# Optimization experiments

Hardware: AMD Instinct MI355X
Metric: run time of the kernel (lower is better)

The kernel has to match this reference:

```python
import jax, jax.numpy as jnp
import numpy as np

B, T, F_DIM, HID, CH = 16, 4096, 47, 64, 256  # batch, frames, feature_dim, hidden_feature_dim, num_channels


def setup_inputs() -> dict:
    key = jax.random.key(0)
    ks = jax.random.split(key, 8)
    s = 0.08  # weight scale
    return {
        "features": jax.random.normal(ks[0], (B, T, F_DIM), jnp.float32),
        # conv1: Conv1d(47, 64, k=1) -> pointwise linear, torch weight (out,in,1) squeezed
        "W1": jax.random.normal(ks[1], (HID, F_DIM), jnp.float32) * s,
        "b1": jnp.zeros((HID,), jnp.float32),
        # conv2: Conv1d(256, 256, k=2), torch weight (out, in, k)
        "W2": jax.random.normal(ks[2], (CH, 4 * HID, 2), jnp.float32) * s,
        "b2": jnp.zeros((CH,), jnp.float32),
        # tconv: ConvTranspose1d(256, 256, k=4, stride=4), torch weight (in, out, k)
        "Wt": jax.random.normal(ks[3], (CH, CH, 4), jnp.float32) * s,
        "bt": jnp.zeros((CH,), jnp.float32),
        # GRU(256, 256), torch layout: (3*H, in) with gate order [r, z, n]
        "W_ih": jax.random.normal(ks[4], (3 * CH, CH), jnp.float32) * s,
        "W_hh": jax.random.normal(ks[5], (3 * CH, CH), jnp.float32) * s,
        "b_ih": jnp.zeros((3 * CH,), jnp.float32),
        "b_hh": jnp.zeros((3 * CH,), jnp.float32),
    }


def reference(features, W1, b1, W2, b2, Wt, bt, W_ih, W_hh, b_ih, b_hh):
    b, t = features.shape[0], features.shape[1]
    ch = Wt.shape[1]
    # conv1 (k=1) == pointwise linear + tanh: (B,T,47) -> (B,T,64)
    c = jnp.tanh(jnp.einsum('btf,hf->bth', features, W1) + b1)
    # group 4 frames: (B, T/4, 256)
    c = c.reshape(b, t // 4, -1)
    # conv2 k=2 with left pad 1 (causal): y[t] = W2[..0] x[t-1] + W2[..1] x[t]
    cp = jnp.pad(c, ((0, 0), (1, 0), (0, 0)))
    c = jnp.tanh(jnp.einsum('bti,oi->bto', cp[:, :-1], W2[:, :, 0])
                 + jnp.einsum('bti,oi->bto', cp[:, 1:], W2[:, :, 1]) + b2)
    # tconv: stride-4 transpose conv, k=4 -> each frame emits 4 steps
    c = jnp.tanh(jnp.einsum('bti,iok->btko', c, Wt) + bt)  # (B, T/4, 4, CH)
    c = c.reshape(b, t, ch)
    # GRU (torch semantics, gate order r,z,n); precompute input projections
    gates_x = jnp.einsum('btc,gc->btg', c, W_ih) + b_ih  # (B,T,3CH)

    def step(h, gx):
        gh = h @ W_hh.T + b_hh
        xr, xz, xn = jnp.split(gx, 3, axis=-1)
        hr, hz, hn = jnp.split(gh, 3, axis=-1)
        r = jax.nn.sigmoid(xr + hr)
        z = jax.nn.sigmoid(xz + hz)
        n = jnp.tanh(xn + r * hn)
        h = (1 - z) * n + z * h
        return h, h

    h0 = jnp.zeros((b, ch), features.dtype)
    _, hs = jax.lax.scan(step, h0, jnp.swapaxes(gates_x, 0, 1))  # (T,B,CH)
    return jnp.swapaxes(hs, 0, 1)  # (B,T,CH)
```

## Files before the change

kernel.cpp:

```cpp
#include <hip/hip_runtime.h>
#include <hip/hip_bf16.h>
#include <stdint.h>

#define B_   16
#define T_   4096
#define F_   47
#define HID_ 64
#define CH_  256
#define TG_  1024
#define G3_  768

using bf16x8 = __attribute__((ext_vector_type(8))) short;
using f32x4  = __attribute__((ext_vector_type(4))) float;
using f16x8  = __attribute__((ext_vector_type(8))) _Float16;

__device__ __forceinline__ short f2bf(float f) {
    union { float f; uint32_t u; } v; v.f = f;
    uint32_t u = v.u;
    uint32_t r = (u + 0x7fffu + ((u >> 16) & 1u)) >> 16;
    return (short)r;
}
__device__ __forceinline__ float bf2f(short s) {
    union { uint32_t u; float f; } v; v.u = ((uint32_t)(uint16_t)s) << 16;
    return v.f;
}
__device__ __forceinline__ float fast_tanh(float x) {
    float e = __expf(2.f * x);
    return 1.f - 2.f / (e + 1.f);
}
__device__ __forceinline__ float fast_sigmoid(float x) {
    return 1.f / (1.f + __expf(-x));
}

#if __has_builtin(__builtin_amdgcn_global_load_lds)
#define HAS_GLL 1
__device__ __forceinline__ void gl_lds16(const void* g, void* l) {
    __builtin_amdgcn_global_load_lds(
        (const __attribute__((address_space(1))) uint32_t*)g,
        (__attribute__((address_space(3))) uint32_t*)l, 16, 0, 0);
}
#else
#define HAS_GLL 0
#endif

__global__ __launch_bounds__(256) void k1_conv1(const float* __restrict__ feat,
        const float* __restrict__ W1, const float* __restrict__ b1,
        short* __restrict__ c1) {
    __shared__ float sW[47 * 64];
    __shared__ float sF[4 * 47];
    int tid = threadIdx.x;
    int b = blockIdx.x >> 10, t0 = (blockIdx.x & 1023) * 4;
    if (tid < 188) sF[tid] = feat[((size_t)b * T_ + t0) * 47 + tid];
    for (int i = tid; i < 47 * 64; i += 256) {
        int f = i >> 6, h = i & 63;
        sW[i] = W1[h * 47 + f];
    }
    __syncthreads();
    int fr = tid >> 6, h = tid & 63;
    float acc = b1[h];
    #pragma unroll
    for (int f = 0; f < 47; ++f)
        acc += sF[fr * 47 + f] * sW[f * 64 + h];
    c1[((size_t)b * T_ + t0 + fr) * 64 + h] = f2bf(fast_tanh(acc));
}

__global__ __launch_bounds__(256) void k_prep(const float* __restrict__ W2,
        const float* __restrict__ Wt, const float* __restrict__ Wih_f,
        short* __restrict__ W2t, short* __restrict__ Wtt, short* __restrict__ Wih) {
    int idx = blockIdx.x * 256 + threadIdx.x;
    if (idx < 256 * 512) {
        int o = idx >> 9, i = idx & 511, d = i >> 8, jj = i & 255;
        W2t[idx] = f2bf(W2[(size_t)o * 512 + jj * 2 + d]);
    }
    {
        int n = idx >> 8, ic = idx & 255, o = n & 255, kp = n >> 8;
        Wtt[idx] = f2bf(Wt[(size_t)ic * 1024 + o * 4 + kp]);
    }
    if (idx < G3_ * CH_)
        Wih[idx] = f2bf(Wih_f[idx]);
}

__global__ __launch_bounds__(256) void k2_conv2(const short* __restrict__ c1,
        const short* __restrict__ W2t, const float* __restrict__ b2,
        short* __restrict__ y2) {
    int tid = threadIdx.x, w = tid >> 6, l = tid & 63;
    int lane16 = l & 15, quad = l >> 4;
    int mt = blockIdx.x * 4 + w;
    int row = mt * 16 + lane16;
    int tg = row & 1023;
    const short* Arow = c1 + (size_t)row * 256 - 256;
    bf16x8 zero8 = {0,0,0,0,0,0,0,0};
    bf16x8 af[16];
    #pragma unroll
    for (int kt = 0; kt < 16; ++kt) {
        int i0 = kt * 32 + quad * 8;
        bool masked = (tg == 0) && (kt < 8);
        const short* p = masked ? c1 : (Arow + i0);
        bf16x8 v = *(const bf16x8*)p;
        af[kt] = masked ? zero8 : v;
    }
    #pragma unroll
    for (int nt = 0; nt < 16; ++nt) {
        int n = nt * 16 + lane16;
        f32x4 acc = {0.f, 0.f, 0.f, 0.f};
        const short* Brow = W2t + (size_t)n * 512 + quad * 8;
        #pragma unroll
        for (int kt = 0; kt < 16; ++kt) {
            bf16x8 bf = *(const bf16x8*)(Brow + kt * 32);
            acc = __builtin_amdgcn_mfma_f32_16x16x32_bf16(af[kt], bf, acc, 0, 0, 0);
        }
        float bias = b2[n];
        #pragma unroll
        for (int r = 0; r < 4; ++r) {
            int mrow = mt * 16 + quad * 4 + r;
            y2[(size_t)mrow * 256 + n] = f2bf(fast_tanh(acc[r] + bias));
        }
    }
}

__global__ __launch_bounds__(256) void k3a_tconv(const short* __restrict__ y2,
        const short* __restrict__ Wtt, const float* __restrict__ bt,
        short* __restrict__ c3) {
    int tid = threadIdx.x, w = tid >> 6, l = tid & 63;
    int lane16 = l & 15, quad = l >> 4;
    int mt = blockIdx.x;
    int row = mt * 16 + lane16;
    const short* Arow = y2 + (size_t)row * 256 + quad * 8;
    bf16x8 af[8];
    #pragma unroll
    for (int kt = 0; kt < 8; ++kt) af[kt] = *(const bf16x8*)(Arow + kt * 32);
    #pragma unroll
    for (int nt2 = 0; nt2 < 16; ++nt2) {
        int n = (w * 16 + nt2) * 16 + lane16;
        f32x4 acc = {0.f, 0.f, 0.f, 0.f};
        const short* Brow = Wtt + (size_t)n * 256 + quad * 8;
        #pragma unroll
        for (int kt = 0; kt < 8; ++kt) {
            bf16x8 bf = *(const bf16x8*)(Brow + kt * 32);
            acc = __builtin_amdgcn_mfma_f32_16x16x32_bf16(af[kt], bf, acc, 0, 0, 0);
        }
        int kp = n >> 8, o = n & 255;
        float bias = bt[o];
        #pragma unroll
        for (int r = 0; r < 4; ++r) {
            int mrow = mt * 16 + quad * 4 + r;
            int bb = mrow >> 10, tgg = mrow & 1023;
            c3[(((size_t)bb * TG_ + tgg) * 4 + kp) * 256 + o] =
                f2bf(fast_tanh(acc[r] + bias));
        }
    }
}

__global__ __launch_bounds__(256) void k3b_xproj(const short* __restrict__ c3,
        const short* __restrict__ Wih, const float* __restrict__ b_ih,
        short* __restrict__ gates) {
    int tid = threadIdx.x, w = tid >> 6, l = tid & 63;
    int lane16 = l & 15, quad = l >> 4;
    int mt = blockIdx.x;
    int row = mt * 16 + lane16;
    const short* Arow = c3 + (size_t)row * 256 + quad * 8;
    bf16x8 af[8];
    #pragma unroll
    for (int kt = 0; kt < 8; ++kt) af[kt] = *(const bf16x8*)(Arow + kt * 32);
    #pragma unroll
    for (int nt2 = 0; nt2 < 12; ++nt2) {
        int n = (w * 12 + nt2) * 16 + lane16;
        f32x4 acc = {0.f, 0.f, 0.f, 0.f};
        const short* Brow = Wih + (size_t)n * 256 + quad * 8;
        #pragma unroll
        for (int kt = 0; kt < 8; ++kt) {
            bf16x8 bf = *(const bf16x8*)(Brow + kt * 32);
            acc = __builtin_amdgcn_mfma_f32_16x16x32_bf16(af[kt], bf, acc, 0, 0, 0);
        }
        float bias = b_ih[n];
        #pragma unroll
        for (int r = 0; r < 4; ++r) {
            int mrow = mt * 16 + quad * 4 + r;
            gates[(size_t)mrow * G3_ + n] = f2bf(acc[r] + bias);
        }
    }
}

__global__ __launch_bounds__(512, 2) void k4_gru_mfma(const float* __restrict__ W_hh,
        const float* __restrict__ b_hh, const short* __restrict__ gates,
        float* __restrict__ out) {
    __shared__ __align__(16) short gxb[2][8][G3_];
    __shared__ __align__(16) float part[G3_];
    __shared__ __align__(16) float ob[8 * 256];
    __shared__ __align__(16) _Float16 h_s[256];

    int tid = threadIdx.x, l = tid & 63, w = tid >> 6;
    int lane16 = l & 15, quad = l >> 4;
    int b = blockIdx.x;

    f16x8 frag[6][8];
    #pragma unroll
    for (int mt = 0; mt < 6; ++mt) {
        const float* wrow = W_hh + (size_t)((w * 6 + mt) * 16 + lane16) * 256 + quad * 8;
        #pragma unroll
        for (int kt = 0; kt < 8; ++kt) {
            const float4* p = (const float4*)(wrow + kt * 32);
            float4 x = p[0], y = p[1];
            f16x8 f;
            f[0] = (_Float16)x.x; f[1] = (_Float16)x.y;
            f[2] = (_Float16)x.z; f[3] = (_Float16)x.w;
            f[4] = (_Float16)y.x; f[5] = (_Float16)y.y;
            f[6] = (_Float16)y.z; f[7] = (_Float16)y.w;
            frag[mt][kt] = f;
        }
    }

    float h_reg = 0.f, bhr = 0.f, bhz = 0.f, bhn = 0.f;
    if (tid < 256) {
        bhr = b_hh[tid]; bhz = b_hh[256 + tid]; bhn = b_hh[512 + tid];
        h_s[tid] = (_Float16)0.f;
    }

    const short* gbase = gates + (size_t)b * T_ * G3_;
    const char* gbytes = (const char*)gbase;

#if HAS_GLL
    {
        char* dst = (char*)&gxb[0][0][0];
        gl_lds16(gbytes + w * 1024 + l * 16, dst + w * 1024);
        if (w < 4) gl_lds16(gbytes + (8 + w) * 1024 + l * 16, dst + (8 + w) * 1024);
    }
#else
    {
        const uint32_t* g32 = (const uint32_t*)gbytes;
        uint32_t* d = (uint32_t*)&gxb[0][0][0];
        #pragma unroll
        for (int i = 0; i < 6; ++i) d[tid + i * 512] = g32[tid + i * 512];
    }
#endif
    __syncthreads();

    float* outb = out + (size_t)b * T_ * CH_;
    for (int s = 0; s < T_; ++s) {
        bool grp0 = ((s & 7) == 0) && (s + 8 < T_);
#if HAS_GLL
        if (grp0) {
            const char* src = gbytes + (size_t)(s + 8) * 1536;
            char* dst = (char*)&gxb[((s >> 3) + 1) & 1][0][0];
            gl_lds16(src + w * 1024 + l * 16, dst + w * 1024);
            if (w < 4) gl_lds16(src + (8 + w) * 1024 + l * 16, dst + (8 + w) * 1024);
        }
#else
        uint32_t pf[6];
        if (grp0) {
            const uint32_t* src = (const uint32_t*)(gbytes + (size_t)(s + 8) * 1536);
            #pragma unroll
            for (int i = 0; i < 6; ++i) pf[i] = src[tid + i * 512];
        }
#endif

        f32x4 acc[6];
        #pragma unroll
        for (int mt = 0; mt < 6; ++mt) acc[mt] = (f32x4){0.f, 0.f, 0.f, 0.f};
        #pragma unroll
        for (int kt = 0; kt < 8; ++kt) {
            f16x8 hb = *(const f16x8*)&h_s[kt * 32 + quad * 8];
            #pragma unroll
            for (int mt = 0; mt < 6; ++mt)
                acc[mt] = __builtin_amdgcn_mfma_f32_16x16x32_f16(frag[mt][kt], hb, acc[mt], 0, 0, 0);
        }
        if (lane16 == 0) {
            #pragma unroll
            for (int mt = 0; mt < 6; ++mt)
                *(f32x4*)&part[(w * 6 + mt) * 16 + quad * 4] = acc[mt];
        }
        __syncthreads();

#if !HAS_GLL
        if (grp0) {
            uint32_t* d = (uint32_t*)&gxb[((s >> 3) + 1) & 1][0][0];
            #pragma unroll
            for (int i = 0; i < 6; ++i) d[tid + i * 512] = pf[i];
        }
#endif
        if (tid < 256) {
            const short* gx = &gxb[(s >> 3) & 1][s & 7][0];
            float gr = part[tid];
            float gz = part[256 + tid];
            float gn = part[512 + tid];
            float xr = bf2f(gx[tid]), xz = bf2f(gx[256 + tid]), xn = bf2f(gx[512 + tid]);
            float r = fast_sigmoid(xr + gr + bhr);
            float z = fast_sigmoid(xz + gz + bhz);
            float nn = fast_tanh(xn + r * (gn + bhn));
            h_reg = (1.f - z) * nn + z * h_reg;
            h_s[tid] = (_Float16)h_reg;
            ob[(s & 7) * 256 + tid] = h_reg;
        }
        __syncthreads();

        if ((s & 7) == 7) {
            f32x4 v = *(const f32x4*)&ob[tid * 4];
            *(f32x4*)&outb[(size_t)(s - 7 + (tid >> 6)) * 256 + (tid & 63) * 4] = v;
        }
    }
}

extern "C" void kernel_launch(void* const* d_in, const int* in_sizes, int n_in,
                              void* d_out, int out_size, void* d_ws, size_t ws_size,
                              hipStream_t stream) {
    const float* feat  = (const float*)d_in[0];
    const float* W1    = (const float*)d_in[1];
    const float* b1    = (const float*)d_in[2];
    const float* W2    = (const float*)d_in[3];
    const float* b2    = (const float*)d_in[4];
    const float* Wt    = (const float*)d_in[5];
    const float* bt    = (const float*)d_in[6];
    const float* Wih_f = (const float*)d_in[7];
    const float* Whh   = (const float*)d_in[8];
    const float* bih   = (const float*)d_in[9];
    const float* bhh   = (const float*)d_in[10];
    float* out = (float*)d_out;

    char* ws = (char*)d_ws;
    short* c3    = (short*)(ws);
    short* c1    = (short*)(ws);
    short* gates = (short*)(ws + 33554432);
    short* y2    = (short*)(ws + 33554432);
    short* W2t   = (short*)(ws + 134217728);
    short* Wtt   = (short*)(ws + 134217728 + 262144);
    short* Wih   = (short*)(ws + 134217728 + 262144 + 524288);

    k1_conv1   <<<16384, 256, 0, stream>>>(feat, W1, b1, c1);
    k_prep     <<<1024, 256, 0, stream>>>(W2, Wt, Wih_f, W2t, Wtt, Wih);
    k2_conv2   <<<256,  256, 0, stream>>>(c1, W2t, b2, y2);
    k3a_tconv  <<<1024, 256, 0, stream>>>(y2, Wtt, bt, c3);
    k3b_xproj  <<<4096, 256, 0, stream>>>(c3, Wih, bih, gates);
    k4_gru_mfma<<<16,   512, 0, stream>>>(Whh, bhh, gates, out);
}
```

Before: 5.763 ms.

## Split GRU recurrent matvec between MFMA (r,z gates) and fdot2 (n gate)

The GRU step kernel now computes only the r and z gate rows of W_hh·h with MFMA, cutting per-wave MFMA tiles from 6 to 4. The n-gate rows are held in registers as packed half2 and computed with fdot2 over quarter-rows, then reduced across 4 lanes with DPP adds. The hidden state moves to a double-buffered, padded LDS layout to avoid bank conflicts and read/write races. The aim is to shorten the serial per-step critical path by splitting the work across MFMA and VALU. In exchange it raises register pressure, which matters at the 512-thread, 2-blocks-per-CU launch bound.

```diff
diff --git a/kernel.cpp b/kernel.cpp
--- a/kernel.cpp
+++ b/kernel.cpp
@@ -13,6 +13,7 @@
 using bf16x8 = __attribute__((ext_vector_type(8))) short;
 using f32x4  = __attribute__((ext_vector_type(4))) float;
 using f16x8  = __attribute__((ext_vector_type(8))) _Float16;
+using h2     = __attribute__((ext_vector_type(2))) _Float16;
 
 __device__ __forceinline__ short f2bf(float f) {
     union { float f; uint32_t u; } v; v.f = f;
@@ -30,6 +31,23 @@
 }
 __device__ __forceinline__ float fast_sigmoid(float x) {
     return 1.f / (1.f + __expf(-x));
+}
+
+#if __has_builtin(__builtin_amdgcn_fdot2)
+#define FDOT2(a, b, c) __builtin_amdgcn_fdot2((a), (b), (c), false)
+#else
+__device__ __forceinline__ float fdot2_emul(h2 a, h2 b, float c) {
+    return c + (float)a[0] * (float)b[0] + (float)a[1] * (float)b[1];
+}
+#define FDOT2(a, b, c) fdot2_emul((a), (b), (c))
+#endif
+
+template <int CTRL>
+__device__ __forceinline__ float dpp_add(float x) {
+    union { float f; int i; } a, b;
+    a.f = x;
+    b.i = __builtin_amdgcn_update_dpp(0, a.i, CTRL, 0xf, 0xf, true);
+    return x + b.f;
 }
 
 #if __has_builtin(__builtin_amdgcn_global_load_lds)
@@ -181,22 +199,23 @@
     }
 }
 
-__global__ __launch_bounds__(512, 2) void k4_gru_mfma(const float* __restrict__ W_hh,
+__global__ __launch_bounds__(512, 2) void k4_gru_hyb(const float* __restrict__ W_hh,
         const float* __restrict__ b_hh, const short* __restrict__ gates,
         float* __restrict__ out) {
     __shared__ __align__(16) short gxb[2][8][G3_];
     __shared__ __align__(16) float part[G3_];
     __shared__ __align__(16) float ob[8 * 256];
-    __shared__ __align__(16) _Float16 h_s[256];
+    __shared__ __align__(16) short hq_s[2][4 * 72];
 
     int tid = threadIdx.x, l = tid & 63, w = tid >> 6;
     int lane16 = l & 15, quad = l >> 4;
+    int q = tid & 3, i2 = tid >> 2;
     int b = blockIdx.x;
 
-    f16x8 frag[6][8];
-    #pragma unroll
-    for (int mt = 0; mt < 6; ++mt) {
-        const float* wrow = W_hh + (size_t)((w * 6 + mt) * 16 + lane16) * 256 + quad * 8;
+    f16x8 afrag[4][8];
+    #pragma unroll
+    for (int mt = 0; mt < 4; ++mt) {
+        const float* wrow = W_hh + (size_t)((w * 4 + mt) * 16 + lane16) * 256 + quad * 8;
         #pragma unroll
         for (int kt = 0; kt < 8; ++kt) {
             const float4* p = (const float4*)(wrow + kt * 32);
@@ -206,15 +225,27 @@
             f[2] = (_Float16)x.z; f[3] = (_Float16)x.w;
             f[4] = (_Float16)y.x; f[5] = (_Float16)y.y;
             f[6] = (_Float16)y.z; f[7] = (_Float16)y.w;
-            frag[mt][kt] = f;
+            afrag[mt][kt] = f;
+        }
+    }
+
+    h2 wreg[2][32];
+    #pragma unroll
+    for (int rr = 0; rr < 2; ++rr) {
+        const float2* row = (const float2*)(W_hh + (size_t)(512 + 2 * i2 + rr) * 256 + q * 64);
+        #pragma unroll
+        for (int j = 0; j < 32; ++j) {
+            float2 v = row[j];
+            h2 p; p[0] = (_Float16)v.x; p[1] = (_Float16)v.y;
+            wreg[rr][j] = p;
         }
     }
 
     float h_reg = 0.f, bhr = 0.f, bhz = 0.f, bhn = 0.f;
     if (tid < 256) {
         bhr = b_hh[tid]; bhz = b_hh[256 + tid]; bhn = b_hh[512 + tid];
-        h_s[tid] = (_Float16)0.f;
-    }
+    }
+    if (tid < 288) hq_s[0][tid] = 0;
 
     const short* gbase = gates + (size_t)b * T_ * G3_;
     const char* gbytes = (const char*)gbase;
@@ -254,20 +285,42 @@
         }
 #endif
 
-        f32x4 acc[6];
-        #pragma unroll
-        for (int mt = 0; mt < 6; ++mt) acc[mt] = (f32x4){0.f, 0.f, 0.f, 0.f};
+        f32x4 acc4[4];
+        #pragma unroll
+        for (int mt = 0; mt < 4; ++mt) acc4[mt] = (f32x4){0.f, 0.f, 0.f, 0.f};
         #pragma unroll
         for (int kt = 0; kt < 8; ++kt) {
-            f16x8 hb = *(const f16x8*)&h_s[kt * 32 + quad * 8];
-            #pragma unroll
-            for (int mt = 0; mt < 6; ++mt)
-                acc[mt] = __builtin_amdgcn_mfma_f32_16x16x32_f16(frag[mt][kt], hb, acc[mt], 0, 0, 0);
-        }
+            int k0 = kt * 32 + quad * 8;
+            f16x8 hb = *(const f16x8*)&hq_s[s & 1][(k0 >> 6) * 72 + (k0 & 63)];
+            #pragma unroll
+            for (int mt = 0; mt < 4; ++mt)
+                acc4[mt] = __builtin_amdgcn_mfma_f32_16x16x32_f16(afrag[mt][kt], hb, acc4[mt], 0, 0, 0);
+        }
+
+        float a0 = 0.f, a1 = 0.f;
+        const short* hb2 = &hq_s[s & 1][q * 72];
+        #pragma unroll
+        for (int g2 = 0; g2 < 8; ++g2) {
+            union { f16x8 v8; h2 p[4]; } hc;
+            hc.v8 = *(const f16x8*)(hb2 + g2 * 8);
+            #pragma unroll
+            for (int p2 = 0; p2 < 4; ++p2) {
+                h2 hv = hc.p[p2];
+                a0 = FDOT2(wreg[0][g2 * 4 + p2], hv, a0);
+                a1 = FDOT2(wreg[1][g2 * 4 + p2], hv, a1);
+            }
+        }
+        a0 = dpp_add<0xB1>(a0); a0 = dpp_add<0x4E>(a0);
+        a1 = dpp_add<0xB1>(a1); a1 = dpp_add<0x4E>(a1);
+
         if (lane16 == 0) {
             #pragma unroll
-            for (int mt = 0; mt < 6; ++mt)
-                *(f32x4*)&part[(w * 6 + mt) * 16 + quad * 4] = acc[mt];
+            for (int mt = 0; mt < 4; ++mt)
+                *(f32x4*)&part[(w * 4 + mt) * 16 + quad * 4] = acc4[mt];
+        }
+        if (q == 0) {
+            float2 nn2; nn2.x = a0; nn2.y = a1;
+            *(float2*)&part[512 + 2 * i2] = nn2;
         }
         __syncthreads();
 
@@ -288,7 +341,8 @@
             float z = fast_sigmoid(xz + gz + bhz);
             float nn = fast_tanh(xn + r * (gn + bhn));
             h_reg = (1.f - z) * nn + z * h_reg;
-            h_s[tid] = (_Float16)h_reg;
+            union { _Float16 f; short u; } cv; cv.f = (_Float16)h_reg;
+            hq_s[(s + 1) & 1][(tid >> 6) * 72 + (tid & 63)] = cv.u;
             ob[(s & 7) * 256 + tid] = h_reg;
         }
         __syncthreads();
@@ -325,10 +379,10 @@
     short* Wtt   = (short*)(ws + 134217728 + 262144);
     short* Wih   = (short*)(ws + 134217728 + 262144 + 524288);
 
-    k1_conv1   <<<16384, 256, 0, stream>>>(feat, W1, b1, c1);
-    k_prep     <<<1024, 256, 0, stream>>>(W2, Wt, Wih_f, W2t, Wtt, Wih);
-    k2_conv2   <<<256,  256, 0, stream>>>(c1, W2t, b2, y2);
-    k3a_tconv  <<<1024, 256, 0, stream>>>(y2, Wtt, bt, c3);
-    k3b_xproj  <<<4096, 256, 0, stream>>>(c3, Wih, bih, gates);
-    k4_gru_mfma<<<16,   512, 0, stream>>>(Whh, bhh, gates, out);
-}
+    k1_conv1  <<<16384, 256, 0, stream>>>(feat, W1, b1, c1);
+    k_prep    <<<1024, 256, 0, stream>>>(W2, Wt, Wih_f, W2t, Wtt, Wih);
+    k2_conv2  <<<256,  256, 0, stream>>>(c1, W2t, b2, y2);
+    k3a_tconv <<<1024, 256, 0, stream>>>(y2, Wtt, bt, c3);
+    k3b_xproj <<<4096, 256, 0, stream>>>(c3, Wih, bih, gates);
+    k4_gru_hyb<<<16,   512, 0, stream>>>(Whh, bhh, gates, out);
+}
```

Result: slower. 6.099 ms (+5.8%).

## Batch all 16 sequences into one GRU block using MFMA N dimension

Applied to the files above, without the earlier changes.

The GRU recurrence now runs in a single 512-thread block that puts the 16 batch elements in the MFMA N dimension, instead of one block per batch where the h vector filled every column. Each lane keeps its gate outputs in registers and applies the nonlinearity directly. This removes the LDS partial-sum round trip and one of the two barriers per step, and h is double-buffered in LDS. Gate inputs are now read straight from global memory every step with no prefetch, and outputs are stored every step, so global latency may land on the serial critical path.

```diff
diff --git a/kernel.cpp b/kernel.cpp
--- a/kernel.cpp
+++ b/kernel.cpp
@@ -11,6 +11,7 @@
 #define G3_  768
 
 using bf16x8 = __attribute__((ext_vector_type(8))) short;
+using bf16x4 = __attribute__((ext_vector_type(4))) short;
 using f32x4  = __attribute__((ext_vector_type(4))) float;
 using f16x8  = __attribute__((ext_vector_type(8))) _Float16;
 
@@ -31,17 +32,15 @@
 __device__ __forceinline__ float fast_sigmoid(float x) {
     return 1.f / (1.f + __expf(-x));
 }
-
-#if __has_builtin(__builtin_amdgcn_global_load_lds)
-#define HAS_GLL 1
-__device__ __forceinline__ void gl_lds16(const void* g, void* l) {
-    __builtin_amdgcn_global_load_lds(
-        (const __attribute__((address_space(1))) uint32_t*)g,
-        (__attribute__((address_space(3))) uint32_t*)l, 16, 0, 0);
-}
-#else
-#define HAS_GLL 0
-#endif
+__device__ __forceinline__ f16x8 cvt8(const float* p) {
+    float4 x = *(const float4*)p, y = *(const float4*)(p + 4);
+    f16x8 f;
+    f[0] = (_Float16)x.x; f[1] = (_Float16)x.y;
+    f[2] = (_Float16)x.z; f[3] = (_Float16)x.w;
+    f[4] = (_Float16)y.x; f[5] = (_Float16)y.y;
+    f[6] = (_Float16)y.z; f[7] = (_Float16)y.w;
+    return f;
+}
 
 __global__ __launch_bounds__(256) void k1_conv1(const float* __restrict__ feat,
         const float* __restrict__ W1, const float* __restrict__ b1,
@@ -181,122 +180,103 @@
     }
 }
 
-__global__ __launch_bounds__(512, 2) void k4_gru_mfma(const float* __restrict__ W_hh,
+__global__ __launch_bounds__(512, 2) void k4_gru_bat(const float* __restrict__ W_hh,
         const float* __restrict__ b_hh, const short* __restrict__ gates,
         float* __restrict__ out) {
-    __shared__ __align__(16) short gxb[2][8][G3_];
-    __shared__ __align__(16) float part[G3_];
-    __shared__ __align__(16) float ob[8 * 256];
-    __shared__ __align__(16) _Float16 h_s[256];
+    __shared__ __align__(16) _Float16 h_s[2][16][264];
 
     int tid = threadIdx.x, l = tid & 63, w = tid >> 6;
-    int lane16 = l & 15, quad = l >> 4;
-    int b = blockIdx.x;
-
-    f16x8 frag[6][8];
-    #pragma unroll
-    for (int mt = 0; mt < 6; ++mt) {
-        const float* wrow = W_hh + (size_t)((w * 6 + mt) * 16 + lane16) * 256 + quad * 8;
+    int bat = l & 15, quad = l >> 4;
+    int chA = w * 16 + quad * 4;
+    int chB = 128 + chA;
+
+    f16x8 aRA[8], aZA[8], aNA[8], aRB[8], aZB[8], aNB[8];
+    {
+        const float* pRA = W_hh + (size_t)(      w * 16 + bat) * 256;
+        const float* pZA = W_hh + (size_t)(256 + w * 16 + bat) * 256;
+        const float* pNA = W_hh + (size_t)(512 + w * 16 + bat) * 256;
+        const float* pRB = W_hh + (size_t)(128 + w * 16 + bat) * 256;
+        const float* pZB = W_hh + (size_t)(384 + w * 16 + bat) * 256;
+        const float* pNB = W_hh + (size_t)(640 + w * 16 + bat) * 256;
         #pragma unroll
         for (int kt = 0; kt < 8; ++kt) {
-            const float4* p = (const float4*)(wrow + kt * 32);
-            float4 x = p[0], y = p[1];
-            f16x8 f;
-            f[0] = (_Float16)x.x; f[1] = (_Float16)x.y;
-            f[2] = (_Float16)x.z; f[3] = (_Float16)x.w;
-            f[4] = (_Float16)y.x; f[5] = (_Float16)y.y;
-            f[6] = (_Float16)y.z; f[7] = (_Float16)y.w;
-            frag[mt][kt] = f;
-        }
-    }
-
-    float h_reg = 0.f, bhr = 0.f, bhz = 0.f, bhn = 0.f;
-    if (tid < 256) {
-        bhr = b_hh[tid]; bhz = b_hh[256 + tid]; bhn = b_hh[512 + tid];
-        h_s[tid] = (_Float16)0.f;
-    }
-
-    const short* gbase = gates + (size_t)b * T_ * G3_;
-    const char* gbytes = (const char*)gbase;
-
-#if HAS_GLL
+            int off = kt * 32 + quad * 8;
+            aRA[kt] = cvt8(pRA + off);
+            aZA[kt] = cvt8(pZA + off);
+            aNA[kt] = cvt8(pNA + off);
+            aRB[kt] = cvt8(pRB + off);
+            aZB[kt] = cvt8(pZB + off);
+            aNB[kt] = cvt8(pNB + off);
+        }
+    }
+
+    f32x4 bRA = *(const f32x4*)(b_hh + chA);
+    f32x4 bZA = *(const f32x4*)(b_hh + 256 + chA);
+    f32x4 bNA = *(const f32x4*)(b_hh + 512 + chA);
+    f32x4 bRB = *(const f32x4*)(b_hh + chB);
+    f32x4 bZB = *(const f32x4*)(b_hh + 256 + chB);
+    f32x4 bNB = *(const f32x4*)(b_hh + 512 + chB);
+
+    f32x4 hA = {0.f, 0.f, 0.f, 0.f}, hB = {0.f, 0.f, 0.f, 0.f};
+
     {
-        char* dst = (char*)&gxb[0][0][0];
-        gl_lds16(gbytes + w * 1024 + l * 16, dst + w * 1024);
-        if (w < 4) gl_lds16(gbytes + (8 + w) * 1024 + l * 16, dst + (8 + w) * 1024);
-    }
-#else
-    {
-        const uint32_t* g32 = (const uint32_t*)gbytes;
-        uint32_t* d = (uint32_t*)&gxb[0][0][0];
-        #pragma unroll
-        for (int i = 0; i < 6; ++i) d[tid + i * 512] = g32[tid + i * 512];
-    }
-#endif
+        short* hz = (short*)&h_s[0][0][0];
+        for (int i = tid; i < 16 * 264; i += 512) hz[i] = 0;
+    }
     __syncthreads();
 
-    float* outb = out + (size_t)b * T_ * CH_;
+    const short* gp = gates + (size_t)bat * T_ * G3_;
+    float* op = out + (size_t)bat * T_ * CH_;
+
     for (int s = 0; s < T_; ++s) {
-        bool grp0 = ((s & 7) == 0) && (s + 8 < T_);
-#if HAS_GLL
-        if (grp0) {
-            const char* src = gbytes + (size_t)(s + 8) * 1536;
-            char* dst = (char*)&gxb[((s >> 3) + 1) & 1][0][0];
-            gl_lds16(src + w * 1024 + l * 16, dst + w * 1024);
-            if (w < 4) gl_lds16(src + (8 + w) * 1024 + l * 16, dst + (8 + w) * 1024);
-        }
-#else
-        uint32_t pf[6];
-        if (grp0) {
-            const uint32_t* src = (const uint32_t*)(gbytes + (size_t)(s + 8) * 1536);
-            #pragma unroll
-            for (int i = 0; i < 6; ++i) pf[i] = src[tid + i * 512];
-        }
-#endif
-
-        f32x4 acc[6];
-        #pragma unroll
-        for (int mt = 0; mt < 6; ++mt) acc[mt] = (f32x4){0.f, 0.f, 0.f, 0.f};
+        const short* g0 = gp + (size_t)s * G3_;
+        bf16x4 gra = *(const bf16x4*)(g0 + chA);
+        bf16x4 gza = *(const bf16x4*)(g0 + 256 + chA);
+        bf16x4 gna = *(const bf16x4*)(g0 + 512 + chA);
+        bf16x4 grb = *(const bf16x4*)(g0 + chB);
+        bf16x4 gzb = *(const bf16x4*)(g0 + 256 + chB);
+        bf16x4 gnb = *(const bf16x4*)(g0 + 512 + chB);
+
+        const _Float16* hrow = &h_s[s & 1][bat][0];
+        f32x4 accRA = {0.f,0.f,0.f,0.f}, accZA = {0.f,0.f,0.f,0.f},
+              accNA = {0.f,0.f,0.f,0.f}, accRB = {0.f,0.f,0.f,0.f},
+              accZB = {0.f,0.f,0.f,0.f}, accNB = {0.f,0.f,0.f,0.f};
         #pragma unroll
         for (int kt = 0; kt < 8; ++kt) {
-            f16x8 hb = *(const f16x8*)&h_s[kt * 32 + quad * 8];
-            #pragma unroll
-            for (int mt = 0; mt < 6; ++mt)
-                acc[mt] = __builtin_amdgcn_mfma_f32_16x16x32_f16(frag[mt][kt], hb, acc[mt], 0, 0, 0);
-        }
-        if (lane16 == 0) {
-            #pragma unroll
-            for (int mt = 0; mt < 6; ++mt)
-                *(f32x4*)&part[(w * 6 + mt) * 16 + quad * 4] = acc[mt];
-        }
+            f16x8 hb = *(const f16x8*)(hrow + kt * 32 + quad * 8);
+            accRA = __builtin_amdgcn_mfma_f32_16x16x32_f16(aRA[kt], hb, accRA, 0, 0, 0);
+            accZA = __builtin_amdgcn_mfma_f32_16x16x32_f16(aZA[kt], hb, accZA, 0, 0, 0);
+            accNA = __builtin_amdgcn_mfma_f32_16x16x32_f16(aNA[kt], hb, accNA, 0, 0, 0);
+            accRB = __builtin_amdgcn_mfma_f32_16x16x32_f16(aRB[kt], hb, accRB, 0, 0, 0);
+            accZB = __builtin_amdgcn_mfma_f32_16x16x32_f16(aZB[kt], hb, accZB, 0, 0, 0);
+            accNB = __builtin_amdgcn_mfma_f32_16x16x32_f16(aNB[kt], hb, accNB, 0, 0, 0);
+        }
+
+        union { _Float16 h4[4]; uint64_t u8; } hpA, hpB;
+        f32x4 ovA, ovB;
+        #pragma unroll
+        for (int r = 0; r < 4; ++r) {
+            float rr = fast_sigmoid(bf2f(gra[r]) + accRA[r] + bRA[r]);
+            float zz = fast_sigmoid(bf2f(gza[r]) + accZA[r] + bZA[r]);
+            float nn = fast_tanh(bf2f(gna[r]) + rr * (accNA[r] + bNA[r]));
+            float hv = (1.f - zz) * nn + zz * hA[r];
+            hA[r] = hv; hpA.h4[r] = (_Float16)hv; ovA[r] = hv;
+
+            float rr2 = fast_sigmoid(bf2f(grb[r]) + accRB[r] + bRB[r]);
+            float zz2 = fast_sigmoid(bf2f(gzb[r]) + accZB[r] + bZB[r]);
+            float nn2 = fast_tanh(bf2f(gnb[r]) + rr2 * (accNB[r] + bNB[r]));
+            float hv2 = (1.f - zz2) * nn2 + zz2 * hB[r];
+            hB[r] = hv2; hpB.h4[r] = (_Float16)hv2; ovB[r] = hv2;
+        }
+        _Float16* hn = &h_s[(s + 1) & 1][bat][0];
+        *(uint64_t*)(hn + chA) = hpA.u8;
+        *(uint64_t*)(hn + chB) = hpB.u8;
+
+        float* o0 = op + (size_t)s * CH_;
+        *(f32x4*)(o0 + chA) = ovA;
+        *(f32x4*)(o0 + chB) = ovB;
+
         __syncthreads();
-
-#if !HAS_GLL
-        if (grp0) {
-            uint32_t* d = (uint32_t*)&gxb[((s >> 3) + 1) & 1][0][0];
-            #pragma unroll
-            for (int i = 0; i < 6; ++i) d[tid + i * 512] = pf[i];
-        }
-#endif
-        if (tid < 256) {
-            const short* gx = &gxb[(s >> 3) & 1][s & 7][0];
-            float gr = part[tid];
-            float gz = part[256 + tid];
-            float gn = part[512 + tid];
-            float xr = bf2f(gx[tid]), xz = bf2f(gx[256 + tid]), xn = bf2f(gx[512 + tid]);
-            float r = fast_sigmoid(xr + gr + bhr);
-            float z = fast_sigmoid(xz + gz + bhz);
-            float nn = fast_tanh(xn + r * (gn + bhn));
-            h_reg = (1.f - z) * nn + z * h_reg;
-            h_s[tid] = (_Float16)h_reg;
-            ob[(s & 7) * 256 + tid] = h_reg;
-        }
-        __syncthreads();
-
-        if ((s & 7) == 7) {
-            f32x4 v = *(const f32x4*)&ob[tid * 4];
-            *(f32x4*)&outb[(size_t)(s - 7 + (tid >> 6)) * 256 + (tid & 63) * 4] = v;
-        }
     }
 }
 
@@ -325,10 +305,10 @@
     short* Wtt   = (short*)(ws + 134217728 + 262144);
     short* Wih   = (short*)(ws + 134217728 + 262144 + 524288);
 
-    k1_conv1   <<<16384, 256, 0, stream>>>(feat, W1, b1, c1);
-    k_prep     <<<1024, 256, 0, stream>>>(W2, Wt, Wih_f, W2t, Wtt, Wih);
-    k2_conv2   <<<256,  256, 0, stream>>>(c1, W2t, b2, y2);
-    k3a_tconv  <<<1024, 256, 0, stream>>>(y2, Wtt, bt, c3);
-    k3b_xproj  <<<4096, 256, 0, stream>>>(c3, Wih, bih, gates);
-    k4_gru_mfma<<<16,   512, 0, stream>>>(Whh, bhh, gates, out);
-}
+    k1_conv1  <<<16384, 256, 0, stream>>>(feat, W1, b1, c1);
+    k_prep    <<<1024, 256, 0, stream>>>(W2, Wt, Wih_f, W2t, Wtt, Wih);
+    k2_conv2  <<<256,  256, 0, stream>>>(c1, W2t, b2, y2);
+    k3a_tconv <<<1024, 256, 0, stream>>>(y2, Wtt, bt, c3);
+    k3b_xproj <<<4096, 256, 0, stream>>>(c3, Wih, bih, gates);
+    k4_gru_bat<<<1,    512, 0, stream>>>(Whh, bhh, gates, out);
+}
```

Result: slower. 20.31 ms (+252.5%).
